# Kernel optimization log

Hardware: AMD Instinct MI355X
Metric: run time of the kernel (lower is better)

The kernel has to match this reference:

```python
import jax, jax.numpy as jnp
import numpy as np

B, S, D = 4, 2048, 1024
H, K = 16, 64
NUM_WINDOW = 8
LN_EPS = 1e-3  # keras LayerNormalization default epsilon


def _mha(x, Wq, bq, Wk, bk, Wv, bv, Wo, bo):
    # x: [b, s, D]; Wq/Wk/Wv: [D, H, K]; Wo: [H, K, D]
    q = jnp.einsum('bsd,dhk->bshk', x, Wq) + bq
    k = jnp.einsum('bsd,dhk->bshk', x, Wk) + bk
    v = jnp.einsum('bsd,dhk->bshk', x, Wv) + bv
    scores = jnp.einsum('bqhk,bshk->bhqs', q, k) / jnp.sqrt(jnp.asarray(K, q.dtype))
    attn = jax.nn.softmax(scores, axis=-1)
    o = jnp.einsum('bhqs,bshk->bqhk', attn, v)
    return jnp.einsum('bqhk,hkd->bqd', o, Wo) + bo


def setup_inputs() -> dict:
    key = jax.random.key(0)
    ks = jax.random.split(key, 20)
    sc = 0.02
    def proj(k):
        return jax.random.normal(k, (D, H, K), jnp.float32) * sc
    inp = {
        'x': jax.random.normal(ks[0], (B, S, D), jnp.float32),
        # global MHA params
        'gWq': proj(ks[1]), 'gbq': jnp.zeros((H, K), jnp.float32),
        'gWk': proj(ks[2]), 'gbk': jnp.zeros((H, K), jnp.float32),
        'gWv': proj(ks[3]), 'gbv': jnp.zeros((H, K), jnp.float32),
        'gWo': jax.random.normal(ks[4], (H, K, D), jnp.float32) * sc,
        'gbo': jnp.zeros((D,), jnp.float32),
        # local MHA params (shared across all windows)
        'lWq': proj(ks[5]), 'lbq': jnp.zeros((H, K), jnp.float32),
        'lWk': proj(ks[6]), 'lbk': jnp.zeros((H, K), jnp.float32),
        'lWv': proj(ks[7]), 'lbv': jnp.zeros((H, K), jnp.float32),
        'lWo': jax.random.normal(ks[8], (H, K, D), jnp.float32) * sc,
        'lbo': jnp.zeros((D,), jnp.float32),
        # layernorm params
        'gamma': jnp.ones((D,), jnp.float32),
        'beta': jnp.zeros((D,), jnp.float32),
    }
    return inp


def reference(x, gWq, gbq, gWk, gbk, gWv, gbv, gWo, gbo,
              lWq, lbq, lWk, lbk, lWv, lbv, lWo, lbo, gamma, beta):
    # global full self-attention
    g_out = _mha(x, gWq, gbq, gWk, gbk, gWv, gbv, gWo, gbo)
    # local windowed self-attention: split seq into NUM_WINDOW blocks; all
    # windows share the same local_mha weights, so fold windows into batch.
    w = S // NUM_WINDOW
    xw = x.reshape(B * NUM_WINDOW, w, D)
    l_out = _mha(xw, lWq, lbq, lWk, lbk, lWv, lbv, lWo, lbo).reshape(B, S, D)
    # residual add of all three streams, then layernorm
    y = x + g_out + l_out
    mu = jnp.mean(y, axis=-1, keepdims=True)
    var = jnp.mean(jnp.square(y - mu), axis=-1, keepdims=True)
    return (y - mu) * jax.lax.rsqrt(var + LN_EPS) * gamma + beta
```

## Files before the change

kernel.cpp:

```cpp
#include <hip/hip_runtime.h>
#include <hip/hip_bf16.h>
#include <type_traits>

using bf16 = __hip_bfloat16;
typedef __bf16 bf16x8 __attribute__((ext_vector_type(8)));
typedef float f32x4 __attribute__((ext_vector_type(4)));
typedef float f32x16 __attribute__((ext_vector_type(16)));
typedef unsigned short u16x8 __attribute__((ext_vector_type(8)));
typedef unsigned int u32;
typedef unsigned int u32x4 __attribute__((ext_vector_type(4)));

#define LOG2E 1.4426950408889634f

static __device__ __forceinline__ unsigned short f2bf_bits(float f) {
  bf16 h = __float2bfloat16(f);
  return __builtin_bit_cast(unsigned short, h);
}

__global__ __launch_bounds__(256) void wtr_kernel(const float* __restrict__ W,
                                                  bf16* __restrict__ out,
                                                  int out_ld, int r_off) {
  __shared__ float tile[32][33];
  int tx = threadIdx.x & 31, ty = threadIdx.x >> 5;
  int c0 = blockIdx.x * 32, r0 = blockIdx.y * 32;
#pragma unroll
  for (int i = 0; i < 4; ++i)
    tile[ty + i * 8][tx] = W[(size_t)(r0 + ty + i * 8) * 1024 + c0 + tx];
  __syncthreads();
#pragma unroll
  for (int i = 0; i < 4; ++i) {
    int cr = ty + i * 8;
    out[(size_t)(c0 + cr) * out_ld + r_off + r0 + tx] = __float2bfloat16(tile[tx][cr]);
  }
}

__global__ void biascat_kernel(const float* gbq, const float* gbk, const float* gbv,
                               const float* lbq, const float* lbk, const float* lbv,
                               const float* gbo, const float* lbo,
                               float* bqkv, float* bo) {
  int i = blockIdx.x * 256 + threadIdx.x;
  if (i < 1024) {
    bqkv[i] = gbq[i];
    bqkv[1024 + i] = gbk[i];
    bqkv[2048 + i] = gbv[i];
    bqkv[3072 + i] = lbq[i];
    bqkv[4096 + i] = lbk[i];
    bqkv[5120 + i] = lbv[i];
    bo[i] = gbo[i] + lbo[i];
  }
}

__global__ __launch_bounds__(256) void castx_kernel(const float* __restrict__ x,
                                                    unsigned short* __restrict__ xb) {
  size_t i = (size_t)blockIdx.x * 256 + threadIdx.x;
  float4 v = reinterpret_cast<const float4*>(x)[i];
  ushort4 o = make_ushort4(f2bf_bits(v.x), f2bf_bits(v.y), f2bf_bits(v.z), f2bf_bits(v.w));
  reinterpret_cast<ushort4*>(xb)[i] = o;
}

template <typename OutT>
__global__ __launch_bounds__(256) void gemm_bt_kernel(
    const bf16* __restrict__ A, const bf16* __restrict__ Bt,
    OutT* __restrict__ C, const float* __restrict__ bias,
    int M, int N, int Kd) {
  __shared__ unsigned short lA[128 * 64];
  __shared__ unsigned short lB[128 * 64];
  const int tid = threadIdx.x;
  const int lane = tid & 63;
  const int wv = tid >> 6;
  const int g = lane >> 4, r15 = lane & 15;
  const int nbx = N >> 7;
  const int nwg = gridDim.x;
  const int bid = blockIdx.x;
  const int wg = (bid & 7) * (nwg >> 3) + (bid >> 3);
  const int tR = (wg / nbx) << 7;
  const int tC = (wg % nbx) << 7;
  const int wr = wv >> 1, wc = wv & 1;

  f32x4 acc[4][4] = {};

  const int srow = lane >> 3;
  const int scol = ((lane & 7) ^ (lane >> 3)) << 3;

  const bf16* Ab = A + (size_t)tR * Kd;
  const bf16* Bb = Bt + (size_t)tC * Kd;

  const int nk = Kd >> 6;
  for (int kt = 0; kt < nk; ++kt) {
    const int k0 = kt << 6;
#pragma unroll
    for (int i = 0; i < 4; ++i) {
      const int c = i * 4 + wv;
      const bf16* gA = Ab + (size_t)(c * 8 + srow) * Kd + (k0 + scol);
      __builtin_amdgcn_global_load_lds(
          (const __attribute__((address_space(1))) unsigned int*)gA,
          (__attribute__((address_space(3))) unsigned int*)&lA[c * 512], 16, 0, 0);
      const bf16* gB = Bb + (size_t)(c * 8 + srow) * Kd + (k0 + scol);
      __builtin_amdgcn_global_load_lds(
          (const __attribute__((address_space(1))) unsigned int*)gB,
          (__attribute__((address_space(3))) unsigned int*)&lB[c * 512], 16, 0, 0);
    }
    __syncthreads();
#pragma unroll
    for (int kk = 0; kk < 2; ++kk) {
      bf16x8 af[4], bfr[4];
#pragma unroll
      for (int m = 0; m < 4; ++m) {
        int row = (wr << 6) + (m << 4) + r15;
        int byt = row * 128 + (((kk << 6) + (g << 4)) ^ ((row & 7) << 4));
        af[m] = *reinterpret_cast<const bf16x8*>((const char*)lA + byt);
      }
#pragma unroll
      for (int n = 0; n < 4; ++n) {
        int row = (wc << 6) + (n << 4) + r15;
        int byt = row * 128 + (((kk << 6) + (g << 4)) ^ ((row & 7) << 4));
        bfr[n] = *reinterpret_cast<const bf16x8*>((const char*)lB + byt);
      }
#pragma unroll
      for (int m = 0; m < 4; ++m)
#pragma unroll
        for (int n = 0; n < 4; ++n)
          acc[m][n] = __builtin_amdgcn_mfma_f32_16x16x32_bf16(af[m], bfr[n], acc[m][n], 0, 0, 0);
    }
    __syncthreads();
  }

#pragma unroll
  for (int n = 0; n < 4; ++n) {
    const int col = tC + (wc << 6) + (n << 4) + r15;
    const float bv = bias ? bias[col] : 0.0f;
#pragma unroll
    for (int m = 0; m < 4; ++m) {
      const int row0 = tR + (wr << 6) + (m << 4) + (g << 2);
#pragma unroll
      for (int j = 0; j < 4; ++j) {
        float v = acc[m][n][j] + bv;
        if constexpr (std::is_same<OutT, float>::value)
          C[(size_t)(row0 + j) * N + col] = v;
        else
          C[(size_t)(row0 + j) * N + col] = __float2bfloat16(v);
      }
    }
  }
}

__global__ __launch_bounds__(256) void vtr_kernel(const bf16* __restrict__ qkv,
                                                  bf16* __restrict__ vt, int colOff) {
  __shared__ unsigned short t[64][72];
  const int tid = threadIdx.x;
  const int s0 = blockIdx.x * 64, h = blockIdx.y, b = blockIdx.z;
  const int sr = tid >> 3, d0 = (tid & 7) * 8;
  const bf16* src = qkv + colOff + h * 64;
#pragma unroll
  for (int p = 0; p < 2; ++p) {
    int s = sr + p * 32;
    u16x8 v = *reinterpret_cast<const u16x8*>(src + (size_t)(b * 2048 + s0 + s) * 6144 + d0);
    *reinterpret_cast<u16x8*>(&t[s][d0]) = v;
  }
  __syncthreads();
  bf16* dst = vt + (size_t)((b * 16 + h) * 64) * 2048 + s0;
#pragma unroll
  for (int p = 0; p < 2; ++p) {
    int d = sr + p * 32;
    u16x8 o;
#pragma unroll
    for (int i = 0; i < 8; ++i) o[i] = t[d0 + i][d];
    *reinterpret_cast<u16x8*>(dst + (size_t)d * 2048 + d0) = o;
  }
}

__global__ __launch_bounds__(256, 3) void attn_kernel(
    const bf16* __restrict__ qkv, const bf16* __restrict__ vt,
    bf16* __restrict__ outp, int qOff, int kOff, int oOff, int isLocal) {
  __shared__ unsigned short lK[2][64 * 64];
  __shared__ unsigned short lV[2][64 * 64];
  const int ldq = 6144;
  const int tid = threadIdx.x, lane = tid & 63, wv = tid >> 6;
  const int q31 = lane & 31, hi = lane >> 5;
  const int qb = blockIdx.x, h = blockIdx.y, b = blockIdx.z;
  const int q0 = qb * 128 + wv * 32;

  const int srow = lane >> 3;
  const int scol = ((lane & 7) ^ (lane >> 3)) << 3;

  const bf16* qp = qkv + (size_t)(b * 2048 + q0 + q31) * ldq + qOff + h * 64 + hi * 8;
  bf16x8 qf0 = *reinterpret_cast<const bf16x8*>(qp);
  bf16x8 qf1 = *reinterpret_cast<const bf16x8*>(qp + 16);
  bf16x8 qf2 = *reinterpret_cast<const bf16x8*>(qp + 32);
  bf16x8 qf3 = *reinterpret_cast<const bf16x8*>(qp + 48);

  const int t0 = isLocal ? ((qb >> 1) << 2) : 0;
  const int nt = isLocal ? 4 : 32;

  const bf16* Kb = qkv + kOff + h * 64;
  const bf16* Vb = vt + (size_t)((b * 16 + h) * 64) * 2048;

  auto stage = [&](int t, int buf) {
    const int krow0 = b * 2048 + t * 64;
#pragma unroll
    for (int i = 0; i < 2; ++i) {
      const int c = i * 4 + wv;
      const int row = c * 8 + srow;
      const bf16* gK = Kb + (size_t)(krow0 + row) * ldq + scol;
      __builtin_amdgcn_global_load_lds(
          (const __attribute__((address_space(1))) unsigned int*)gK,
          (__attribute__((address_space(3))) unsigned int*)&lK[buf][c * 512], 16, 0, 0);
      const bf16* gV = Vb + (size_t)row * 2048 + t * 64 + scol;
      __builtin_amdgcn_global_load_lds(
          (const __attribute__((address_space(1))) unsigned int*)gV,
          (__attribute__((address_space(3))) unsigned int*)&lV[buf][c * 512], 16, 0, 0);
    }
  };

  float mrun = -1e30f;
  f32x16 accO0 = {}, accO1 = {}, accL = {};
  const float C8 = 0.125f * LOG2E;
  const u32x4 onep = {0x3F803F80u, 0x3F803F80u, 0x3F803F80u, 0x3F803F80u};
  const bf16x8 onesA = __builtin_bit_cast(bf16x8, onep);

  stage(t0, 0);

  auto body = [&](int tt, auto bufc) {
    constexpr int BUF = decltype(bufc)::value;
    __syncthreads();
    if (tt + 1 < nt) stage(t0 + tt + 1, BUF ^ 1);

    f32x16 s0 = {}, s1 = {};
    const char* lkb = (const char*)&lK[BUF][0];
#pragma unroll
    for (int kap = 0; kap < 4; ++kap) {
      bf16x8 qf = kap == 0 ? qf0 : kap == 1 ? qf1 : kap == 2 ? qf2 : qf3;
      {
        const int row = q31;
        bf16x8 kf = *reinterpret_cast<const bf16x8*>(
            lkb + row * 128 + ((kap * 32 + hi * 16) ^ ((row & 7) << 4)));
        s0 = __builtin_amdgcn_mfma_f32_32x32x16_bf16(kf, qf, s0, 0, 0, 0);
      }
      {
        const int row = 32 + q31;
        bf16x8 kf = *reinterpret_cast<const bf16x8*>(
            lkb + row * 128 + ((kap * 32 + hi * 16) ^ ((row & 7) << 4)));
        s1 = __builtin_amdgcn_mfma_f32_32x32x16_bf16(kf, qf, s1, 0, 0, 0);
      }
    }

    float t16[16];
#pragma unroll
    for (int i = 0; i < 16; ++i) t16[i] = fmaxf(s0[i], s1[i]);
#pragma unroll
    for (int st = 8; st; st >>= 1)
#pragma unroll
      for (int i = 0; i < st; ++i) t16[i] = fmaxf(t16[i], t16[i + st]);
    float m2 = fmaxf(t16[0], __shfl_xor(t16[0], 32));
    if (__any(m2 > mrun + 64.0f)) {
      float mn = fmaxf(mrun, m2);
      float ascl = exp2f((mrun - mn) * C8);
      mrun = mn;
      accO0 *= ascl;
      accO1 *= ascl;
      accL *= ascl;
    }
    const float nm = -mrun * C8;
#pragma unroll
    for (int i = 0; i < 16; ++i) s0[i] = exp2f(fmaf(s0[i], C8, nm));
#pragma unroll
    for (int i = 0; i < 16; ++i) s1[i] = exp2f(fmaf(s1[i], C8, nm));

    u32 W0[8], W1[8];
#pragma unroll
    for (int m = 0; m < 4; ++m)
#pragma unroll
      for (int u = 0; u < 2; ++u) {
        asm("v_cvt_pk_bf16_f32 %0, %1, %2"
            : "=v"(W0[m * 2 + u])
            : "v"(s0[m * 4 + 2 * u]), "v"(s0[m * 4 + 2 * u + 1]));
        asm("v_cvt_pk_bf16_f32 %0, %1, %2"
            : "=v"(W1[m * 2 + u])
            : "v"(s1[m * 4 + 2 * u]), "v"(s1[m * 4 + 2 * u + 1]));
      }

    const char* lvb = (const char*)&lV[BUF][0];
#define PV_BLOCK(Wb, KAP)                                                          \
  {                                                                                \
    u32 w0 = Wb[(((KAP) & 1) * 2) * 2 + 0], w1 = Wb[(((KAP) & 1) * 2) * 2 + 1];    \
    u32 w2 = Wb[(((KAP) & 1) * 2 + 1) * 2 + 0], w3 = Wb[(((KAP) & 1) * 2 + 1) * 2 + 1]; \
    asm("v_permlane32_swap_b32 %0, %1" : "+v"(w0), "+v"(w2));                      \
    asm("v_permlane32_swap_b32 %0, %1" : "+v"(w1), "+v"(w3));                      \
    bf16x8 pa = __builtin_bit_cast(bf16x8, (u32x4){w0, w1, w2, w3});               \
    {                                                                              \
      const int row = q31;                                                         \
      bf16x8 vf = *reinterpret_cast<const bf16x8*>(                                \
          lvb + row * 128 + (((KAP) * 32 + hi * 16) ^ ((row & 7) << 4)));          \
      accO0 = __builtin_amdgcn_mfma_f32_32x32x16_bf16(vf, pa, accO0, 0, 0, 0);     \
    }                                                                              \
    {                                                                              \
      const int row = 32 + q31;                                                    \
      bf16x8 vf = *reinterpret_cast<const bf16x8*>(                                \
          lvb + row * 128 + (((KAP) * 32 + hi * 16) ^ ((row & 7) << 4)));          \
      accO1 = __builtin_amdgcn_mfma_f32_32x32x16_bf16(vf, pa, accO1, 0, 0, 0);     \
    }                                                                              \
    accL = __builtin_amdgcn_mfma_f32_32x32x16_bf16(onesA, pa, accL, 0, 0, 0);      \
  }
    PV_BLOCK(W0, 0)
    PV_BLOCK(W0, 1)
    PV_BLOCK(W1, 2)
    PV_BLOCK(W1, 3)
#undef PV_BLOCK
  };

  for (int tt = 0; tt < nt; tt += 2) {
    body(tt, std::integral_constant<int, 0>{});
    body(tt + 1, std::integral_constant<int, 1>{});
  }

  const float inv = 1.0f / accL[0];
  bf16* orow = outp + (size_t)(b * 2048 + q0 + q31) * 2048 + oOff + h * 64;
#pragma unroll
  for (int rg = 0; rg < 4; ++rg) {
    const int d0 = 8 * rg + 4 * hi;
    ushort4 o0 = make_ushort4(f2bf_bits(accO0[4 * rg + 0] * inv), f2bf_bits(accO0[4 * rg + 1] * inv),
                              f2bf_bits(accO0[4 * rg + 2] * inv), f2bf_bits(accO0[4 * rg + 3] * inv));
    *reinterpret_cast<ushort4*>(orow + d0) = o0;
    ushort4 o1 = make_ushort4(f2bf_bits(accO1[4 * rg + 0] * inv), f2bf_bits(accO1[4 * rg + 1] * inv),
                              f2bf_bits(accO1[4 * rg + 2] * inv), f2bf_bits(accO1[4 * rg + 3] * inv));
    *reinterpret_cast<ushort4*>(orow + 32 + d0) = o1;
  }
}

__global__ __launch_bounds__(256) void ln_kernel(const float* __restrict__ x,
                                                 const float* __restrict__ ygl,
                                                 const float* __restrict__ gamma,
                                                 const float* __restrict__ beta,
                                                 float* __restrict__ out) {
  const int row = blockIdx.x, t = threadIdx.x, lane = t & 63, wv = t >> 6;
  __shared__ float red[8];
  const float4* xr = reinterpret_cast<const float4*>(x + (size_t)row * 1024);
  const float4* yr = reinterpret_cast<const float4*>(ygl + (size_t)row * 1024);
  float4 a = xr[t], c = yr[t];
  float y0 = a.x + c.x, y1 = a.y + c.y, y2 = a.z + c.z, y3 = a.w + c.w;
  float s = y0 + y1 + y2 + y3;
#pragma unroll
  for (int o = 32; o; o >>= 1) s += __shfl_down(s, o);
  if (!lane) red[wv] = s;
  __syncthreads();
  float mu = (red[0] + red[1] + red[2] + red[3]) * (1.f / 1024.f);
  float d0 = y0 - mu, d1 = y1 - mu, d2 = y2 - mu, d3 = y3 - mu;
  float q = d0 * d0 + d1 * d1 + d2 * d2 + d3 * d3;
#pragma unroll
  for (int o = 32; o; o >>= 1) q += __shfl_down(q, o);
  if (!lane) red[4 + wv] = q;
  __syncthreads();
  float var = (red[4] + red[5] + red[6] + red[7]) * (1.f / 1024.f);
  float r = rsqrtf(var + 1e-3f);
  float4 gm = reinterpret_cast<const float4*>(gamma)[t];
  float4 bt = reinterpret_cast<const float4*>(beta)[t];
  float4 o4;
  o4.x = d0 * r * gm.x + bt.x;
  o4.y = d1 * r * gm.y + bt.y;
  o4.z = d2 * r * gm.z + bt.z;
  o4.w = d3 * r * gm.w + bt.w;
  reinterpret_cast<float4*>(out + (size_t)row * 1024)[t] = o4;
}

extern "C" void kernel_launch(void* const* d_in, const int* in_sizes, int n_in,
                              void* d_out, int out_size, void* d_ws, size_t ws_size,
                              hipStream_t stream) {
  const float* x = (const float*)d_in[0];
  const float* gWq = (const float*)d_in[1];
  const float* gbq = (const float*)d_in[2];
  const float* gWk = (const float*)d_in[3];
  const float* gbk = (const float*)d_in[4];
  const float* gWv = (const float*)d_in[5];
  const float* gbv = (const float*)d_in[6];
  const float* gWo = (const float*)d_in[7];
  const float* gbo = (const float*)d_in[8];
  const float* lWq = (const float*)d_in[9];
  const float* lbq = (const float*)d_in[10];
  const float* lWk = (const float*)d_in[11];
  const float* lbk = (const float*)d_in[12];
  const float* lWv = (const float*)d_in[13];
  const float* lbv = (const float*)d_in[14];
  const float* lWo = (const float*)d_in[15];
  const float* lbo = (const float*)d_in[16];
  const float* gamma = (const float*)d_in[17];
  const float* beta = (const float*)d_in[18];
  float* out = (float*)d_out;

  char* ws = (char*)d_ws;
  size_t off = 0;
  auto alloc = [&](size_t bytes) {
    void* p = ws + off;
    off += (bytes + 255) & ~(size_t)255;
    return p;
  };
  bf16* xb = (bf16*)alloc((size_t)8192 * 1024 * 2);
  bf16* Wt = (bf16*)alloc((size_t)6144 * 1024 * 2);
  bf16* WoT = (bf16*)alloc((size_t)1024 * 2048 * 2);
  float* bQKV = (float*)alloc(6144 * 4);
  float* bO = (float*)alloc(1024 * 4);
  bf16* QKV = (bf16*)alloc((size_t)8192 * 6144 * 2);
  bf16* Vtg = (bf16*)alloc((size_t)64 * 64 * 2048 * 2);
  bf16* Vtl = (bf16*)alloc((size_t)64 * 64 * 2048 * 2);
  bf16* OgOl = (bf16*)alloc((size_t)8192 * 2048 * 2);
  float* ygl = (float*)QKV;

  dim3 blk(256);
  wtr_kernel<<<dim3(32, 32), blk, 0, stream>>>(gWq, Wt + (size_t)0 * 1024 * 1024, 1024, 0);
  wtr_kernel<<<dim3(32, 32), blk, 0, stream>>>(gWk, Wt + (size_t)1 * 1024 * 1024, 1024, 0);
  wtr_kernel<<<dim3(32, 32), blk, 0, stream>>>(gWv, Wt + (size_t)2 * 1024 * 1024, 1024, 0);
  wtr_kernel<<<dim3(32, 32), blk, 0, stream>>>(lWq, Wt + (size_t)3 * 1024 * 1024, 1024, 0);
  wtr_kernel<<<dim3(32, 32), blk, 0, stream>>>(lWk, Wt + (size_t)4 * 1024 * 1024, 1024, 0);
  wtr_kernel<<<dim3(32, 32), blk, 0, stream>>>(lWv, Wt + (size_t)5 * 1024 * 1024, 1024, 0);
  wtr_kernel<<<dim3(32, 32), blk, 0, stream>>>(gWo, WoT, 2048, 0);
  wtr_kernel<<<dim3(32, 32), blk, 0, stream>>>(lWo, WoT, 2048, 1024);
  biascat_kernel<<<dim3(4), blk, 0, stream>>>(gbq, gbk, gbv, lbq, lbk, lbv, gbo, lbo, bQKV, bO);
  castx_kernel<<<dim3(8192), blk, 0, stream>>>(x, (unsigned short*)xb);
  gemm_bt_kernel<bf16><<<dim3(64 * 48), blk, 0, stream>>>(xb, Wt, QKV, bQKV, 8192, 6144, 1024);
  vtr_kernel<<<dim3(32, 16, 4), blk, 0, stream>>>(QKV, Vtg, 2048);
  vtr_kernel<<<dim3(32, 16, 4), blk, 0, stream>>>(QKV, Vtl, 5120);
  attn_kernel<<<dim3(16, 16, 4), blk, 0, stream>>>(QKV, Vtg, OgOl, 0, 1024, 0, 0);
  attn_kernel<<<dim3(16, 16, 4), blk, 0, stream>>>(QKV, Vtl, OgOl, 3072, 4096, 1024, 1);
  gemm_bt_kernel<float><<<dim3(64 * 8), blk, 0, stream>>>(OgOl, WoT, ygl, bO, 8192, 1024, 2048);
  ln_kernel<<<dim3(8192), blk, 0, stream>>>(x, ygl, gamma, beta, out);
}
```

Measured before the change: 516.0 us.

## Use 256x256-tile 8-wave pipelined GEMM for the fused QKV projection

Replaces the 128x128 QKV projection GEMM with a 256x256 tile kernel using 512 threads, a double-buffered 128KB LDS ring, and staged quarter-tile prefetches interleaved with MFMA phases. The phases are bracketed by barriers and s_setprio to overlap global-to-LDS loads with matrix math. The larger tile raises arithmetic intensity per byte loaded, but the 128KB of LDS per workgroup limits occupancy. It also depends on explicit vmcnt bookkeeping being correct.

```diff
diff --git a/kernel.cpp b/kernel.cpp
--- a/kernel.cpp
+++ b/kernel.cpp
@@ -11,6 +11,11 @@
 typedef unsigned int u32x4 __attribute__((ext_vector_type(4)));
 
 #define LOG2E 1.4426950408889634f
+
+#define GLDS16(gptr, lptr)                                                  \
+  __builtin_amdgcn_global_load_lds(                                         \
+      (const __attribute__((address_space(1))) unsigned int*)(gptr),        \
+      (__attribute__((address_space(3))) unsigned int*)(lptr), 16, 0, 0)
 
 static __device__ __forceinline__ unsigned short f2bf_bits(float f) {
   bf16 h = __float2bfloat16(f);
@@ -56,6 +61,157 @@
   float4 v = reinterpret_cast<const float4*>(x)[i];
   ushort4 o = make_ushort4(f2bf_bits(v.x), f2bf_bits(v.y), f2bf_bits(v.z), f2bf_bits(v.w));
   reinterpret_cast<ushort4*>(xb)[i] = o;
+}
+
+__global__ __launch_bounds__(512, 2) void gemm256_kernel(
+    const bf16* __restrict__ A, const bf16* __restrict__ Bt,
+    bf16* __restrict__ C, const float* __restrict__ bias,
+    int M, int N, int Kd) {
+  __shared__ unsigned short lds[65536];
+  const int tid = threadIdx.x, lane = tid & 63, wv = tid >> 6;
+  const int g = lane >> 4, r15 = lane & 15;
+  const int wr = wv >> 2, wc = wv & 3;
+  const int nbx = N >> 8;
+  const int nwg = gridDim.x;
+  const int bid = blockIdx.x;
+  const int wg = (bid & 7) * (nwg >> 3) + (bid >> 3);
+  const int tR = (wg / nbx) << 8;
+  const int tC = (wg % nbx) << 8;
+
+  const int srow = lane >> 3;
+  const int scol = ((lane & 7) ^ srow) << 3;
+  const int nt = Kd >> 6;
+
+  const bf16* Ab = A + (size_t)tR * Kd;
+  const bf16* Bb = Bt + (size_t)tC * Kd;
+
+  auto stageQ = [&](int arr, int half, int kt) {
+    const bf16* gb = (arr ? Bb : Ab) + (size_t)(half * 128) * Kd + kt * 64 + scol;
+    unsigned short* db = &lds[arr * 32768 + (((kt & 1) * 2 + half) * 128) * 64];
+#pragma unroll
+    for (int rd = 0; rd < 2; ++rd)
+      GLDS16(gb + (size_t)(rd * 64 + wv * 8 + srow) * Kd, db + (rd * 64 + wv * 8) * 64);
+  };
+
+  const char* ldsB = (const char*)lds;
+  auto rdA = [&](int buf, int rowInHalf, int kk) -> bf16x8 {
+    int base = ((buf * 2 + wr) * 128 + rowInHalf) * 128;
+    int cb = ((kk << 6) + (g << 4)) ^ ((rowInHalf & 7) << 4);
+    return *reinterpret_cast<const bf16x8*>(ldsB + base + cb);
+  };
+  auto rdB = [&](int buf, int n, int kk) -> bf16x8 {
+    int row = (wc & 1) * 64 + n * 16 + r15;
+    int base = 65536 + ((buf * 2 + (wc >> 1)) * 128 + row) * 128;
+    int cb = ((kk << 6) + (g << 4)) ^ ((row & 7) << 4);
+    return *reinterpret_cast<const bf16x8*>(ldsB + base + cb);
+  };
+
+#define PH_ENTER()                                    \
+  __builtin_amdgcn_sched_barrier(0);                  \
+  __builtin_amdgcn_s_barrier();                       \
+  asm volatile("s_waitcnt lgkmcnt(0)" ::: "memory");  \
+  __builtin_amdgcn_sched_barrier(0);                  \
+  __builtin_amdgcn_s_setprio(1)
+#define PH_EXIT()                                     \
+  __builtin_amdgcn_s_setprio(0);                      \
+  __builtin_amdgcn_sched_barrier(0);                  \
+  __builtin_amdgcn_s_barrier()
+
+  f32x4 acc[8][4] = {};
+  bf16x8 aF[4][2], bFa[2][2], bFb[2][2];
+
+  stageQ(1, 0, 0);
+  stageQ(1, 1, 0);
+  stageQ(0, 0, 0);
+  stageQ(0, 1, 0);
+  if (nt > 1) {
+    stageQ(1, 0, 1);
+    stageQ(1, 1, 1);
+    asm volatile("s_waitcnt vmcnt(4)" ::: "memory");
+  } else {
+    asm volatile("s_waitcnt vmcnt(0)" ::: "memory");
+  }
+  __builtin_amdgcn_s_barrier();
+
+  for (int t = 0; t < nt; ++t) {
+    const int buf = t & 1;
+#pragma unroll
+    for (int m = 0; m < 4; ++m)
+#pragma unroll
+      for (int kk = 0; kk < 2; ++kk) aF[m][kk] = rdA(buf, m * 16 + r15, kk);
+#pragma unroll
+    for (int n = 0; n < 2; ++n)
+#pragma unroll
+      for (int kk = 0; kk < 2; ++kk) bFa[n][kk] = rdB(buf, n, kk);
+    if (t + 1 < nt) stageQ(0, 0, t + 1);
+    PH_ENTER();
+#pragma unroll
+    for (int m = 0; m < 4; ++m)
+#pragma unroll
+      for (int n = 0; n < 2; ++n)
+#pragma unroll
+        for (int kk = 0; kk < 2; ++kk)
+          acc[m][n] = __builtin_amdgcn_mfma_f32_16x16x32_bf16(aF[m][kk], bFa[n][kk], acc[m][n], 0, 0, 0);
+    PH_EXIT();
+#pragma unroll
+    for (int n = 0; n < 2; ++n)
+#pragma unroll
+      for (int kk = 0; kk < 2; ++kk) bFb[n][kk] = rdB(buf, 2 + n, kk);
+    if (t + 1 < nt) stageQ(0, 1, t + 1);
+    PH_ENTER();
+#pragma unroll
+    for (int m = 0; m < 4; ++m)
+#pragma unroll
+      for (int n = 0; n < 2; ++n)
+#pragma unroll
+        for (int kk = 0; kk < 2; ++kk)
+          acc[m][2 + n] = __builtin_amdgcn_mfma_f32_16x16x32_bf16(aF[m][kk], bFb[n][kk], acc[m][2 + n], 0, 0, 0);
+    PH_EXIT();
+#pragma unroll
+    for (int m = 0; m < 4; ++m)
+#pragma unroll
+      for (int kk = 0; kk < 2; ++kk) aF[m][kk] = rdA(buf, 64 + m * 16 + r15, kk);
+    if (t + 2 < nt) stageQ(1, 0, t + 2);
+    PH_ENTER();
+#pragma unroll
+    for (int m = 0; m < 4; ++m)
+#pragma unroll
+      for (int n = 0; n < 2; ++n)
+#pragma unroll
+        for (int kk = 0; kk < 2; ++kk)
+          acc[4 + m][2 + n] = __builtin_amdgcn_mfma_f32_16x16x32_bf16(aF[m][kk], bFb[n][kk], acc[4 + m][2 + n], 0, 0, 0);
+    PH_EXIT();
+    if (t + 2 < nt) {
+      stageQ(1, 1, t + 2);
+      asm volatile("s_waitcnt vmcnt(4)" ::: "memory");
+    } else {
+      asm volatile("s_waitcnt vmcnt(0)" ::: "memory");
+    }
+    PH_ENTER();
+#pragma unroll
+    for (int m = 0; m < 4; ++m)
+#pragma unroll
+      for (int n = 0; n < 2; ++n)
+#pragma unroll
+        for (int kk = 0; kk < 2; ++kk)
+          acc[4 + m][n] = __builtin_amdgcn_mfma_f32_16x16x32_bf16(aF[m][kk], bFa[n][kk], acc[4 + m][n], 0, 0, 0);
+    PH_EXIT();
+  }
+#undef PH_ENTER
+#undef PH_EXIT
+
+#pragma unroll
+  for (int n = 0; n < 4; ++n) {
+    const int col = tC + wc * 64 + n * 16 + r15;
+    const float bv = bias[col];
+#pragma unroll
+    for (int m = 0; m < 8; ++m) {
+      const int row0 = tR + wr * 128 + m * 16 + (g << 2);
+#pragma unroll
+      for (int j = 0; j < 4; ++j)
+        C[(size_t)(row0 + j) * N + col] = __float2bfloat16(acc[m][n][j] + bv);
+    }
+  }
 }
 
 template <typename OutT>
@@ -92,13 +248,9 @@
     for (int i = 0; i < 4; ++i) {
       const int c = i * 4 + wv;
       const bf16* gA = Ab + (size_t)(c * 8 + srow) * Kd + (k0 + scol);
-      __builtin_amdgcn_global_load_lds(
-          (const __attribute__((address_space(1))) unsigned int*)gA,
-          (__attribute__((address_space(3))) unsigned int*)&lA[c * 512], 16, 0, 0);
+      GLDS16(gA, &lA[c * 512]);
       const bf16* gB = Bb + (size_t)(c * 8 + srow) * Kd + (k0 + scol);
-      __builtin_amdgcn_global_load_lds(
-          (const __attribute__((address_space(1))) unsigned int*)gB,
-          (__attribute__((address_space(3))) unsigned int*)&lB[c * 512], 16, 0, 0);
+      GLDS16(gB, &lB[c * 512]);
     }
     __syncthreads();
 #pragma unroll
@@ -202,13 +354,9 @@
       const int c = i * 4 + wv;
       const int row = c * 8 + srow;
       const bf16* gK = Kb + (size_t)(krow0 + row) * ldq + scol;
-      __builtin_amdgcn_global_load_lds(
-          (const __attribute__((address_space(1))) unsigned int*)gK,
-          (__attribute__((address_space(3))) unsigned int*)&lK[buf][c * 512], 16, 0, 0);
+      GLDS16(gK, &lK[buf][c * 512]);
       const bf16* gV = Vb + (size_t)row * 2048 + t * 64 + scol;
-      __builtin_amdgcn_global_load_lds(
-          (const __attribute__((address_space(1))) unsigned int*)gV,
-          (__attribute__((address_space(3))) unsigned int*)&lV[buf][c * 512], 16, 0, 0);
+      GLDS16(gV, &lV[buf][c * 512]);
     }
   };
 
@@ -415,7 +563,7 @@
   wtr_kernel<<<dim3(32, 32), blk, 0, stream>>>(lWo, WoT, 2048, 1024);
   biascat_kernel<<<dim3(4), blk, 0, stream>>>(gbq, gbk, gbv, lbq, lbk, lbv, gbo, lbo, bQKV, bO);
   castx_kernel<<<dim3(8192), blk, 0, stream>>>(x, (unsigned short*)xb);
-  gemm_bt_kernel<bf16><<<dim3(64 * 48), blk, 0, stream>>>(xb, Wt, QKV, bQKV, 8192, 6144, 1024);
+  gemm256_kernel<<<dim3(32 * 24), dim3(512), 0, stream>>>(xb, Wt, QKV, bQKV, 8192, 6144, 1024);
   vtr_kernel<<<dim3(32, 16, 4), blk, 0, stream>>>(QKV, Vtg, 2048);
   vtr_kernel<<<dim3(32, 16, 4), blk, 0, stream>>>(QKV, Vtl, 5120);
   attn_kernel<<<dim3(16, 16, 4), blk, 0, stream>>>(QKV, Vtg, OgOl, 0, 1024, 0, 0);
```

Measured after the change: 494.9 us. -4.1%, faster.
